# Kernel tuning notes

Measured on AMD Instinct MI355X. Metric: run time of the kernel, lower is better.

The kernel has to match this reference:

```python
import jax, jax.numpy as jnp
import numpy as np
import math

B, S, D = 2, 2048, 2048
P = 4       # num_entangled_pairs
PW = 2      # num_interference_pathways
L = 2       # num_layers
STD = 0.02
EPS = 1e-5


def _layer_norm(x, g, b):
    m = jnp.mean(x, axis=-1, keepdims=True)
    v = jnp.mean(jnp.square(x - m), axis=-1, keepdims=True)
    return (x - m) * jax.lax.rsqrt(v + EPS) * g + b


def setup_inputs() -> dict:
    key = jax.random.key(0)
    ks = jax.random.split(key, 16)
    n = lambda k, shape: jax.random.normal(k, shape, dtype=jnp.float32) * STD
    inp = {
        "x": jax.random.normal(ks[0], (B, S, D), dtype=jnp.float32),
        # superposition layer
        "amp_w": n(ks[1], (D, D)), "amp_b": jnp.zeros((D,), jnp.float32),
        "ph_w": n(ks[2], (D, D)), "ph_b": jnp.zeros((D,), jnp.float32),
        # per-layer entanglement
        "ent_w": n(ks[3], (L, D, P * D)), "ent_b": jnp.zeros((L, P * D), jnp.float32),
        "ent_pw": n(ks[4], (L, P * D, D)), "ent_pb": jnp.zeros((L, D), jnp.float32),
        # per-layer interference pathways
        "path_w": n(ks[5], (L, PW, D, D)), "path_b": jnp.zeros((L, PW, D), jnp.float32),
        "phase": jax.random.normal(ks[6], (L, PW, D), dtype=jnp.float32),
        # layer norms (norm3 / norm4 of each layer)
        "ln3_g": jnp.ones((L, D), jnp.float32), "ln3_b": jnp.zeros((L, D), jnp.float32),
        "ln4_g": jnp.ones((L, D), jnp.float32), "ln4_b": jnp.zeros((L, D), jnp.float32),
    }
    return inp


def reference(x, amp_w, amp_b, ph_w, ph_b, ent_w, ent_b, ent_pw, ent_pb,
              path_w, path_b, phase, ln3_g, ln3_b, ln4_g, ln4_b):
    # QuantumSuperpositionLayer on the input
    amp = jax.nn.sigmoid(x @ amp_w + amp_b)
    ph = jnp.tanh(x @ ph_w + ph_b) * math.pi
    h = (jnp.cos(ph) + jnp.sin(ph)) * amp                      # [B,S,D]

    for l in range(L):
        # QuantumEntanglementLayer: expand to P*D then project back
        e = h @ ent_w[l] + ent_b[l]                            # [B,S,P*D]
        ent = e @ ent_pw[l] + ent_pb[l]                        # [B,S,D]
        h = _layer_norm(h + ent, ln3_g[l], ln3_b[l])

        # QuantumInterferenceLayer: sum over pathways with phase modulation
        t = jnp.einsum('bsd,pdf->pbsf', h, path_w[l]) + path_b[l][:, None, None, :]
        mod = jnp.cos(phase[l]) + jnp.sin(phase[l])            # [PW,D]
        interf = jnp.sum(t * mod[:, None, None, :], axis=0)   # [B,S,D]
        h = _layer_norm(h + interf, ln4_g[l], ln4_b[l])
    return h
```

## Files before the change

### kernel.cpp

```cpp
#include <hip/hip_runtime.h>
#include <cstdint>
#include <cstddef>

typedef unsigned short u16;
typedef short bf16x8 __attribute__((ext_vector_type(8)));
typedef float f32x4 __attribute__((ext_vector_type(4)));

__device__ __forceinline__ float bf2f(u16 v) {
  union { unsigned int u; float f; } x; x.u = ((unsigned int)v) << 16; return x.f;
}
__device__ __forceinline__ u16 f2bf(float f) {
  union { float f; unsigned int u; } x; x.f = f;
  unsigned int r = (x.u + 0x7fffu + ((x.u >> 16) & 1u)) >> 16;
  return (u16)r;
}

__device__ __forceinline__ void async16(const u16* g, u16* lds) {
  __builtin_amdgcn_global_load_lds(
      (const __attribute__((address_space(1))) void*)g,
      (__attribute__((address_space(3))) void*)lds, 16, 0, 0);
}

#define BM 256
#define BN 256
#define BK 64

#define VMW(n) asm volatile("s_waitcnt vmcnt(" #n ")" ::: "memory")
#define BAR() do { asm volatile("" ::: "memory"); \
                   __builtin_amdgcn_s_barrier(); \
                   asm volatile("" ::: "memory"); } while (0)

template <bool ACC>
__global__ __launch_bounds__(512, 2) void gemm_bt(
    const u16* __restrict__ A, int lda,
    const u16* __restrict__ Bt,
    const float* __restrict__ bias,
    u16* __restrict__ C, int ldc,
    int M, int N, int K)
{
  __shared__ __align__(16) u16 As[2][BM * BK];
  __shared__ __align__(16) u16 Bs[2][BN * BK];
  const int tid = threadIdx.x;
  const int w   = tid >> 6;
  const int l   = tid & 63;
  const int wm  = w >> 2;
  const int wn  = w & 3;
  const int tRow = l & 15;
  const int quad = l >> 4;
  const int s7 = tRow & 7;
  const int bm = blockIdx.x, bn = blockIdx.y;

  const int rsub = tid >> 3;
  const int cLog = (tid & 7) ^ (rsub & 7);
  const u16* ag[2][2]; const u16* bg[2][2];
  #pragma unroll
  for (int H = 0; H < 2; ++H) {
    #pragma unroll
    for (int j = 0; j < 2; ++j) {
      const int ra = H * 64 + j * 128 + rsub;
      ag[H][j] = A + (size_t)(bm * BM + ra) * lda + cLog * 8;
      const int p  = j * 64 + rsub;
      const int rb = (p & 31) + H * 32 + (p >> 5) * 64;
      bg[H][j] = Bt + (size_t)(bn * BN + rb) * K + cLog * 8;
    }
  }
  const int ldsW = w * 512;

  f32x4 acc[8][4] = {};
  bf16x8 af[4][2], bf0[2][2], bf1[2][2];

#define STAGE_A(H, NB) do { \
    async16(ag[H][0], &As[NB][(H) * 8192 + ldsW]); \
    async16(ag[H][1], &As[NB][(H) * 8192 + 4096 + ldsW]); \
    ag[H][0] += BK; ag[H][1] += BK; } while (0)
#define STAGE_B(H, NB) do { \
    async16(bg[H][0], &Bs[NB][(H) * 8192 + ldsW]); \
    async16(bg[H][1], &Bs[NB][(H) * 8192 + 4096 + ldsW]); \
    bg[H][0] += BK; bg[H][1] += BK; } while (0)
#define READ_A(CB, H) do { \
    _Pragma("unroll") \
    for (int mt = 0; mt < 4; ++mt) { \
      _Pragma("unroll") \
      for (int kk = 0; kk < 2; ++kk) \
        af[mt][kk] = *(const bf16x8*)&As[CB][(H) * 8192 + \
            (wm * 64 + mt * 16 + tRow) * 64 + (((kk * 4 + quad) ^ s7)) * 8]; \
    } } while (0)
#define READ_B(CB, H, BF) do { \
    _Pragma("unroll") \
    for (int nt = 0; nt < 2; ++nt) { \
      _Pragma("unroll") \
      for (int kk = 0; kk < 2; ++kk) \
        BF[nt][kk] = *(const bf16x8*)&Bs[CB][(H) * 8192 + \
            (wn * 32 + nt * 16 + tRow) * 64 + (((kk * 4 + quad) ^ s7)) * 8]; \
    } } while (0)
#define MFMA_BLK(BF, MI0, NI0) do { \
    __builtin_amdgcn_s_setprio(1); \
    _Pragma("unroll") \
    for (int mt = 0; mt < 4; ++mt) { \
      _Pragma("unroll") \
      for (int nt = 0; nt < 2; ++nt) { \
        _Pragma("unroll") \
        for (int kk = 0; kk < 2; ++kk) \
          acc[(MI0) + mt][(NI0) + nt] = __builtin_amdgcn_mfma_f32_16x16x32_bf16( \
              af[mt][kk], BF[nt][kk], acc[(MI0) + mt][(NI0) + nt], 0, 0, 0); \
      } } \
    __builtin_amdgcn_s_setprio(0); } while (0)

  STAGE_A(0, 0); STAGE_B(0, 0); STAGE_B(1, 0); STAGE_A(1, 0);
  VMW(4);
  BAR();

  const int NT = K / BK;
  for (int u = 0; u < NT - 1; ++u) {
    const int cb = u & 1, nb = cb ^ 1;
    READ_A(cb, 0); READ_B(cb, 0, bf0);
    STAGE_A(0, nb);
    VMW(4); BAR();
    MFMA_BLK(bf0, 0, 0);
    BAR();
    READ_B(cb, 1, bf1);
    STAGE_B(0, nb);
    VMW(4); BAR();
    MFMA_BLK(bf1, 0, 2);
    BAR();
    READ_A(cb, 1);
    STAGE_B(1, nb);
    VMW(4); BAR();
    MFMA_BLK(bf1, 4, 2);
    BAR();
    STAGE_A(1, nb);
    VMW(4); BAR();
    MFMA_BLK(bf0, 4, 0);
    BAR();
  }
  {
    const int cb = (NT - 1) & 1;
    READ_A(cb, 0); READ_B(cb, 0, bf0);
    VMW(2); BAR();
    MFMA_BLK(bf0, 0, 0);
    BAR();
    READ_B(cb, 1, bf1);
    VMW(0); BAR();
    MFMA_BLK(bf1, 0, 2);
    BAR();
    READ_A(cb, 1);
    BAR();
    MFMA_BLK(bf1, 4, 2);
    BAR();
    MFMA_BLK(bf0, 4, 0);
  }
#undef STAGE_A
#undef STAGE_B
#undef READ_A
#undef READ_B
#undef MFMA_BLK

  const int crow0 = bm * BM + wm * 128;
  const int ccol0 = bn * BN + wn * 64;
  #pragma unroll
  for (int ni = 0; ni < 4; ++ni) {
    int col = ccol0 + ni * 16 + tRow;
    float bv = ACC ? 0.f : bias[col];
    #pragma unroll
    for (int mi = 0; mi < 8; ++mi) {
      int r0 = crow0 + mi * 16 + quad * 4;
      #pragma unroll
      for (int r = 0; r < 4; ++r) {
        size_t idx = (size_t)(r0 + r) * ldc + col;
        float v = acc[mi][ni][r] + bv;
        if (ACC) v += bf2f(C[idx]);
        C[idx] = f2bf(v);
      }
    }
  }
}

__global__ __launch_bounds__(256) void transpose_f2bf(
    const float* __restrict__ src, u16* __restrict__ dst,
    int R, int C, int srcStride, int col0)
{
  __shared__ __align__(16) u16 tile[64][72];
  const int bx = blockIdx.x;
  const int by = blockIdx.y;
  const int t = threadIdx.x;
  const int r  = t >> 4;
  const int c4 = (t & 15) * 4;
  #pragma unroll
  for (int i = 0; i < 4; ++i) {
    int row = r + i * 16;
    f32x4 v = *(const f32x4*)&src[(size_t)(by * 64 + row) * srcStride + col0 + bx * 64 + c4];
    #pragma unroll
    for (int j = 0; j < 4; ++j) tile[row][c4 + j] = f2bf(v[j]);
  }
  __syncthreads();
  const int orow0 = t >> 3;
  const int oc8   = (t & 7) * 8;
  #pragma unroll
  for (int i = 0; i < 2; ++i) {
    int orow = orow0 + i * 32;
    u16 tmp[8];
    #pragma unroll
    for (int j = 0; j < 8; ++j) tmp[j] = tile[oc8 + j][orow];
    *(uint4*)&dst[(size_t)(bx * 64 + orow) * R + by * 64 + oc8] = *(uint4*)tmp;
  }
}

__global__ void cvt_f2bf(const float* __restrict__ s, u16* __restrict__ d) {
  size_t i = ((size_t)blockIdx.x * 256 + threadIdx.x) * 8;
  f32x4 a = *(const f32x4*)&s[i];
  f32x4 b = *(const f32x4*)&s[i + 4];
  u16 o[8];
  #pragma unroll
  for (int j = 0; j < 4; ++j) { o[j] = f2bf(a[j]); o[j + 4] = f2bf(b[j]); }
  *(uint4*)&d[i] = *(uint4*)o;
}

__global__ void mod_k(const float* __restrict__ ph, float* __restrict__ m, int n) {
  int i = blockIdx.x * 256 + threadIdx.x;
  if (i < n) { float p = ph[i]; m[i] = cosf(p) + sinf(p); }
}

__global__ void concat2_k(const float* __restrict__ a, const float* __restrict__ b,
                          float* __restrict__ d, int n) {
  int i = blockIdx.x * 256 + threadIdx.x;
  if (i < n) { d[i] = a[i]; d[n + i] = b[i]; }
}

__global__ __launch_bounds__(256) void combine_path_k(
    const float* __restrict__ pw, const float* __restrict__ mod,
    u16* __restrict__ WcT, int D)
{
  __shared__ float tile[64][65];
  const int bx = blockIdx.x;
  const int by = blockIdx.y;
  const int t = threadIdx.x;
  const int r  = t >> 4;
  const int c4 = (t & 15) * 4;
  float acc[4][4];
  #pragma unroll
  for (int i = 0; i < 4; ++i)
    #pragma unroll
    for (int j = 0; j < 4; ++j) acc[i][j] = 0.f;
  for (int p = 0; p < 2; ++p) {
    float m[4];
    #pragma unroll
    for (int j = 0; j < 4; ++j) m[j] = mod[p * D + bx * 64 + c4 + j];
    #pragma unroll
    for (int i = 0; i < 4; ++i) {
      int d = by * 64 + r + i * 16;
      f32x4 v = *(const f32x4*)&pw[((size_t)p * D + d) * D + bx * 64 + c4];
      #pragma unroll
      for (int j = 0; j < 4; ++j) acc[i][j] += v[j] * m[j];
    }
  }
  #pragma unroll
  for (int i = 0; i < 4; ++i)
    #pragma unroll
    for (int j = 0; j < 4; ++j) tile[r + i * 16][c4 + j] = acc[i][j];
  __syncthreads();
  const int fo0 = t >> 3;
  const int oc8 = (t & 7) * 8;
  #pragma unroll
  for (int i = 0; i < 2; ++i) {
    int fo = fo0 + i * 32;
    u16 tmp[8];
    #pragma unroll
    for (int j = 0; j < 8; ++j) tmp[j] = f2bf(tile[oc8 + j][fo]);
    *(uint4*)&WcT[(size_t)(bx * 64 + fo) * D + by * 64 + oc8] = *(uint4*)tmp;
  }
}

__global__ void combine_bias_k(const float* __restrict__ pb, const float* __restrict__ mod,
                               float* __restrict__ bc, int D) {
  int f = blockIdx.x * 256 + threadIdx.x;
  if (f < D) bc[f] = pb[f] * mod[f] + pb[D + f] * mod[D + f];
}

__global__ __launch_bounds__(256) void superpose_k(
    const u16* __restrict__ zc, u16* __restrict__ h, int D)
{
  size_t idx = (size_t)blockIdx.x * 256 + threadIdx.x;
  int grpPerRow = D / 8;
  size_t row = idx / grpPerRow;
  int cg = (int)(idx % grpPerRow);
  size_t zbase = row * (size_t)(2 * D) + cg * 8;
  uint4 v1 = *(const uint4*)&zc[zbase];
  uint4 v2 = *(const uint4*)&zc[zbase + D];
  const u16* p1 = (const u16*)&v1;
  const u16* p2 = (const u16*)&v2;
  u16 o[8];
  #pragma unroll
  for (int j = 0; j < 8; ++j) {
    float a = bf2f(p1[j]);
    float p = bf2f(p2[j]);
    float amp = 1.f / (1.f + __expf(-a));
    float ph = 3.14159265358979323f * tanhf(p);
    float s, c;
    __sincosf(ph, &s, &c);
    o[j] = f2bf((c + s) * amp);
  }
  *(uint4*)&h[row * D + cg * 8] = *(uint4*)o;
}

template <bool F32OUT>
__global__ __launch_bounds__(256) void add_ln_k(
    const u16* __restrict__ hin, const u16* __restrict__ delta,
    const float* __restrict__ g, const float* __restrict__ b,
    void* __restrict__ outp, int D)
{
  const int row = blockIdx.x;
  const int t = threadIdx.x;
  const size_t base = (size_t)row * D;
  uint4 hv = *(const uint4*)&hin[base + t * 8];
  uint4 dv = *(const uint4*)&delta[base + t * 8];
  const u16* hp = (const u16*)&hv;
  const u16* dp = (const u16*)&dv;
  float x[8];
  float s = 0.f, s2 = 0.f;
  #pragma unroll
  for (int j = 0; j < 8; ++j) {
    x[j] = bf2f(hp[j]) + bf2f(dp[j]);
    s += x[j]; s2 += x[j] * x[j];
  }
  #pragma unroll
  for (int o = 32; o > 0; o >>= 1) {
    s  += __shfl_down(s, o, 64);
    s2 += __shfl_down(s2, o, 64);
  }
  __shared__ float ss[4], ss2[4];
  if ((t & 63) == 0) { ss[t >> 6] = s; ss2[t >> 6] = s2; }
  __syncthreads();
  float S  = ss[0] + ss[1] + ss[2] + ss[3];
  float S2 = ss2[0] + ss2[1] + ss2[2] + ss2[3];
  float mean = S / D;
  float var = S2 / D - mean * mean;
  float rstd = rsqrtf(var + 1e-5f);
  float y[8];
  #pragma unroll
  for (int j = 0; j < 8; ++j)
    y[j] = (x[j] - mean) * rstd * g[t * 8 + j] + b[t * 8 + j];
  if constexpr (F32OUT) {
    float* out = (float*)outp;
    f32x4 lo = {y[0], y[1], y[2], y[3]};
    f32x4 hi = {y[4], y[5], y[6], y[7]};
    *(f32x4*)&out[base + t * 8]     = lo;
    *(f32x4*)&out[base + t * 8 + 4] = hi;
  } else {
    u16* out = (u16*)outp;
    u16 o8[8];
    #pragma unroll
    for (int j = 0; j < 8; ++j) o8[j] = f2bf(y[j]);
    *(uint4*)&out[base + t * 8] = *(uint4*)o8;
  }
}

extern "C" void kernel_launch(void* const* d_in, const int* in_sizes, int n_in,
                              void* d_out, int out_size, void* d_ws, size_t ws_size,
                              hipStream_t stream) {
  const float* x      = (const float*)d_in[0];
  const float* amp_w  = (const float*)d_in[1];
  const float* amp_b  = (const float*)d_in[2];
  const float* ph_w   = (const float*)d_in[3];
  const float* ph_b   = (const float*)d_in[4];
  const float* ent_w  = (const float*)d_in[5];
  const float* ent_b  = (const float*)d_in[6];
  const float* ent_pw = (const float*)d_in[7];
  const float* ent_pb = (const float*)d_in[8];
  const float* path_w = (const float*)d_in[9];
  const float* path_b = (const float*)d_in[10];
  const float* phase  = (const float*)d_in[11];
  const float* ln3_g  = (const float*)d_in[12];
  const float* ln3_b  = (const float*)d_in[13];
  const float* ln4_g  = (const float*)d_in[14];
  const float* ln4_b  = (const float*)d_in[15];

  constexpr int D = 2048, PD = 8192, M = 4096, L = 2, PW = 2;
  constexpr int HPD = PD / 2;

  char* p = (char*)d_ws;
  float* modf = (float*)p; p += (size_t)L * PW * D * sizeof(float);
  float* bcf  = (float*)p; p += (size_t)2 * D * sizeof(float);
  p = (char*)d_ws + 65536;
  u16* h  = (u16*)p; p += (size_t)M * D * sizeof(u16);
  u16* t1 = (u16*)p; p += (size_t)M * D * sizeof(u16);
  u16* wT = (u16*)p; p += (size_t)HPD * D * sizeof(u16);
  u16* e  = (u16*)p; p += (size_t)M * PD * sizeof(u16);

  u16* xb = e;
  u16* zc = e + (size_t)M * D;

  dim3 b256(256);
  dim3 b512(512);

  mod_k<<<(L * PW * D) / 256, b256, 0, stream>>>(phase, modf, L * PW * D);
  cvt_f2bf<<<(M * D) / (256 * 8), b256, 0, stream>>>(x, xb);

  transpose_f2bf<<<dim3(D / 64, D / 64), b256, 0, stream>>>(amp_w, wT, D, D, D, 0);
  transpose_f2bf<<<dim3(D / 64, D / 64), b256, 0, stream>>>(ph_w, wT + (size_t)D * D, D, D, D, 0);
  concat2_k<<<D / 256, b256, 0, stream>>>(amp_b, ph_b, bcf, D);
  gemm_bt<false><<<dim3(M / BM, (2 * D) / BN), b512, 0, stream>>>(
      xb, D, wT, bcf, zc, 2 * D, M, 2 * D, D);
  superpose_k<<<(M * D) / (256 * 8), b256, 0, stream>>>(zc, h, D);

  for (int l = 0; l < L; ++l) {
    for (int s = 0; s < 2; ++s) {
      transpose_f2bf<<<dim3(HPD / 64, D / 64), b256, 0, stream>>>(
          ent_w + (size_t)l * D * PD, wT, D, HPD, PD, s * HPD);
      gemm_bt<false><<<dim3(M / BM, HPD / BN), b512, 0, stream>>>(
          h, D, wT, ent_b + (size_t)l * PD + s * HPD, e + s * HPD, PD, M, HPD, D);
    }
    for (int s = 0; s < 2; ++s) {
      transpose_f2bf<<<dim3(D / 64, HPD / 64), b256, 0, stream>>>(
          ent_pw + (size_t)l * PD * D + (size_t)s * HPD * D, wT, HPD, D, D, 0);
      if (s == 0)
        gemm_bt<false><<<dim3(M / BM, D / BN), b512, 0, stream>>>(
            e, PD, wT, ent_pb + (size_t)l * D, t1, D, M, D, HPD);
      else
        gemm_bt<true><<<dim3(M / BM, D / BN), b512, 0, stream>>>(
            e + HPD, PD, wT, bcf , t1, D, M, D, HPD);
    }
    add_ln_k<false><<<M, b256, 0, stream>>>(h, t1, ln3_g + (size_t)l * D, ln3_b + (size_t)l * D, h, D);
    combine_path_k<<<dim3(D / 64, D / 64), b256, 0, stream>>>(
        path_w + (size_t)l * PW * D * D, modf + (size_t)l * PW * D, wT, D);
    combine_bias_k<<<D / 256, b256, 0, stream>>>(path_b + (size_t)l * PW * D, modf + (size_t)l * PW * D, bcf, D);
    gemm_bt<false><<<dim3(M / BM, D / BN), b512, 0, stream>>>(
        h, D, wT, bcf, t1, D, M, D, D);
    if (l == L - 1)
      add_ln_k<true><<<M, b256, 0, stream>>>(h, t1, ln4_g + (size_t)l * D, ln4_b + (size_t)l * D, d_out, D);
    else
      add_ln_k<false><<<M, b256, 0, stream>>>(h, t1, ln4_g + (size_t)l * D, ln4_b + (size_t)l * D, h, D);
  }
}
```

Baseline: 1.511 ms.

## Template GEMM on N-tile width and deepen async prefetch to two tiles ahead

Makes the GEMM tile width a template parameter and uses 128-wide N tiles for the M x 2048 output GEMMs, doubling grid size for better CU occupancy. The main loop is restructured so both LDS buffers are filled in the prologue and each tile's buffer is refilled after it is consumed, keeping two K-tiles of loads in flight with tuned vmcnt waits. Narrower tiles lower arithmetic intensity per block, and the deeper pipeline depends on correct wait counts.

```diff
diff --git a/kernel.cpp b/kernel.cpp
--- a/kernel.cpp
+++ b/kernel.cpp
@@ -21,16 +21,27 @@
       (__attribute__((address_space(3))) void*)lds, 16, 0, 0);
 }
 
-#define BM 256
-#define BN 256
-#define BK 64
-
-#define VMW(n) asm volatile("s_waitcnt vmcnt(" #n ")" ::: "memory")
+template <int N> __device__ __forceinline__ void vmw() {
+  if constexpr (N < 0) {}
+  else if constexpr (N == 0)  asm volatile("s_waitcnt vmcnt(0)" ::: "memory");
+  else if constexpr (N == 2)  asm volatile("s_waitcnt vmcnt(2)" ::: "memory");
+  else if constexpr (N == 3)  asm volatile("s_waitcnt vmcnt(3)" ::: "memory");
+  else if constexpr (N == 4)  asm volatile("s_waitcnt vmcnt(4)" ::: "memory");
+  else if constexpr (N == 6)  asm volatile("s_waitcnt vmcnt(6)" ::: "memory");
+  else if constexpr (N == 8)  asm volatile("s_waitcnt vmcnt(8)" ::: "memory");
+  else if constexpr (N == 9)  asm volatile("s_waitcnt vmcnt(9)" ::: "memory");
+  else if constexpr (N == 10) asm volatile("s_waitcnt vmcnt(10)" ::: "memory");
+  else if constexpr (N == 12) asm volatile("s_waitcnt vmcnt(12)" ::: "memory");
+}
+
 #define BAR() do { asm volatile("" ::: "memory"); \
                    __builtin_amdgcn_s_barrier(); \
                    asm volatile("" ::: "memory"); } while (0)
 
-template <bool ACC>
+#define BM 256
+#define BK 64
+
+template <bool ACC, int BNT>
 __global__ __launch_bounds__(512, 2) void gemm_bt(
     const u16* __restrict__ A, int lda,
     const u16* __restrict__ Bt,
@@ -38,8 +49,14 @@
     u16* __restrict__ C, int ldc,
     int M, int N, int K)
 {
+  constexpr int NIH   = BNT / 128;
+  constexpr int NI    = 2 * NIH;
+  constexpr int JB    = BNT / 128;
+  constexpr int BHALF = BNT * 32;
+
   __shared__ __align__(16) u16 As[2][BM * BK];
-  __shared__ __align__(16) u16 Bs[2][BN * BK];
+  __shared__ __align__(16) u16 Bs[2][BNT * BK];
+
   const int tid = threadIdx.x;
   const int w   = tid >> 6;
   const int l   = tid & 63;
@@ -52,31 +69,35 @@
 
   const int rsub = tid >> 3;
   const int cLog = (tid & 7) ^ (rsub & 7);
-  const u16* ag[2][2]; const u16* bg[2][2];
+  const u16* ag[2][2]; const u16* bg[2][JB];
   #pragma unroll
   for (int H = 0; H < 2; ++H) {
     #pragma unroll
     for (int j = 0; j < 2; ++j) {
       const int ra = H * 64 + j * 128 + rsub;
       ag[H][j] = A + (size_t)(bm * BM + ra) * lda + cLog * 8;
+    }
+    #pragma unroll
+    for (int j = 0; j < JB; ++j) {
       const int p  = j * 64 + rsub;
-      const int rb = (p & 31) + H * 32 + (p >> 5) * 64;
-      bg[H][j] = Bt + (size_t)(bn * BN + rb) * K + cLog * 8;
+      const int rb = (p / (16 * NIH)) * (32 * NIH) + H * (16 * NIH) + (p % (16 * NIH));
+      bg[H][j] = Bt + (size_t)(bn * BNT + rb) * K + cLog * 8;
     }
   }
   const int ldsW = w * 512;
 
-  f32x4 acc[8][4] = {};
-  bf16x8 af[4][2], bf0[2][2], bf1[2][2];
+  f32x4 acc[8][NI] = {};
+  bf16x8 af[4][2], bf0[NIH][2], bf1[NIH][2];
 
 #define STAGE_A(H, NB) do { \
     async16(ag[H][0], &As[NB][(H) * 8192 + ldsW]); \
     async16(ag[H][1], &As[NB][(H) * 8192 + 4096 + ldsW]); \
     ag[H][0] += BK; ag[H][1] += BK; } while (0)
 #define STAGE_B(H, NB) do { \
-    async16(bg[H][0], &Bs[NB][(H) * 8192 + ldsW]); \
-    async16(bg[H][1], &Bs[NB][(H) * 8192 + 4096 + ldsW]); \
-    bg[H][0] += BK; bg[H][1] += BK; } while (0)
+    _Pragma("unroll") \
+    for (int j = 0; j < JB; ++j) { \
+      async16(bg[H][j], &Bs[NB][(H) * BHALF + j * 4096 + ldsW]); \
+      bg[H][j] += BK; } } while (0)
 #define READ_A(CB, H) do { \
     _Pragma("unroll") \
     for (int mt = 0; mt < 4; ++mt) { \
@@ -87,18 +108,18 @@
     } } while (0)
 #define READ_B(CB, H, BF) do { \
     _Pragma("unroll") \
-    for (int nt = 0; nt < 2; ++nt) { \
+    for (int nt = 0; nt < NIH; ++nt) { \
       _Pragma("unroll") \
       for (int kk = 0; kk < 2; ++kk) \
-        BF[nt][kk] = *(const bf16x8*)&Bs[CB][(H) * 8192 + \
-            (wn * 32 + nt * 16 + tRow) * 64 + (((kk * 4 + quad) ^ s7)) * 8]; \
+        BF[nt][kk] = *(const bf16x8*)&Bs[CB][(H) * BHALF + \
+            (wn * 16 * NIH + nt * 16 + tRow) * 64 + (((kk * 4 + quad) ^ s7)) * 8]; \
     } } while (0)
 #define MFMA_BLK(BF, MI0, NI0) do { \
     __builtin_amdgcn_s_setprio(1); \
     _Pragma("unroll") \
     for (int mt = 0; mt < 4; ++mt) { \
       _Pragma("unroll") \
-      for (int nt = 0; nt < 2; ++nt) { \
+      for (int nt = 0; nt < NIH; ++nt) { \
         _Pragma("unroll") \
         for (int kk = 0; kk < 2; ++kk) \
           acc[(MI0) + mt][(NI0) + nt] = __builtin_amdgcn_mfma_f32_16x16x32_bf16( \
@@ -106,49 +127,51 @@
       } } \
     __builtin_amdgcn_s_setprio(0); } while (0)
 
+#define TILE(P0, P1, P3, DOSTAGE) do { \
+    const int cb = u & 1; \
+     \
+    READ_A(cb, 0); READ_B(cb, 0, bf0); \
+    vmw<P0>(); BAR(); \
+    MFMA_BLK(bf0, 0, 0); \
+    BAR(); \
+     \
+    READ_B(cb, 1, bf1); \
+    if (DOSTAGE) { STAGE_A(0, cb); STAGE_B(0, cb); } \
+    vmw<P1>(); BAR(); \
+    MFMA_BLK(bf1, 0, NIH); \
+    BAR(); \
+     \
+    READ_A(cb, 1); \
+    if (DOSTAGE) { STAGE_B(1, cb); } \
+    BAR(); \
+    MFMA_BLK(bf1, 4, NIH); \
+    BAR(); \
+     \
+    if (DOSTAGE) { STAGE_A(1, cb); } \
+    vmw<P3>(); BAR(); \
+    MFMA_BLK(bf0, 4, 0); \
+    BAR(); \
+  } while (0)
+
+  constexpr int PRO = (BNT == 256) ? 12 : 9;
+  constexpr int P0W = (BNT == 256) ? 10 : 8;
+  constexpr int P1W = (BNT == 256) ? 12 : 9;
+  constexpr int P3W = (BNT == 256) ? 12 : 9;
+  constexpr int T1W = (BNT == 256) ? 8 : 6;
+  constexpr int T3W = (BNT == 256) ? 4 : 3;
+
   STAGE_A(0, 0); STAGE_B(0, 0); STAGE_B(1, 0); STAGE_A(1, 0);
-  VMW(4);
+  STAGE_A(0, 1); STAGE_B(0, 1); STAGE_B(1, 1); STAGE_A(1, 1);
+  vmw<PRO>();
   BAR();
 
   const int NT = K / BK;
-  for (int u = 0; u < NT - 1; ++u) {
-    const int cb = u & 1, nb = cb ^ 1;
-    READ_A(cb, 0); READ_B(cb, 0, bf0);
-    STAGE_A(0, nb);
-    VMW(4); BAR();
-    MFMA_BLK(bf0, 0, 0);
-    BAR();
-    READ_B(cb, 1, bf1);
-    STAGE_B(0, nb);
-    VMW(4); BAR();
-    MFMA_BLK(bf1, 0, 2);
-    BAR();
-    READ_A(cb, 1);
-    STAGE_B(1, nb);
-    VMW(4); BAR();
-    MFMA_BLK(bf1, 4, 2);
-    BAR();
-    STAGE_A(1, nb);
-    VMW(4); BAR();
-    MFMA_BLK(bf0, 4, 0);
-    BAR();
-  }
-  {
-    const int cb = (NT - 1) & 1;
-    READ_A(cb, 0); READ_B(cb, 0, bf0);
-    VMW(2); BAR();
-    MFMA_BLK(bf0, 0, 0);
-    BAR();
-    READ_B(cb, 1, bf1);
-    VMW(0); BAR();
-    MFMA_BLK(bf1, 0, 2);
-    BAR();
-    READ_A(cb, 1);
-    BAR();
-    MFMA_BLK(bf1, 4, 2);
-    BAR();
-    MFMA_BLK(bf0, 4, 0);
-  }
+  int u = 0;
+  for (; u < NT - 2; ++u) { TILE(P0W, P1W, P3W, true); }
+  { TILE(P0W, T1W, T3W, false); ++u; }
+  { TILE(2, 0, -1, false); }
+
+#undef TILE
 #undef STAGE_A
 #undef STAGE_B
 #undef READ_A
@@ -156,9 +179,9 @@
 #undef MFMA_BLK
 
   const int crow0 = bm * BM + wm * 128;
-  const int ccol0 = bn * BN + wn * 64;
-  #pragma unroll
-  for (int ni = 0; ni < 4; ++ni) {
+  const int ccol0 = bn * BNT + wn * (NIH * 32);
+  #pragma unroll
+  for (int ni = 0; ni < NI; ++ni) {
     int col = ccol0 + ni * 16 + tRow;
     float bv = ACC ? 0.f : bias[col];
     #pragma unroll
@@ -398,7 +421,7 @@
   transpose_f2bf<<<dim3(D / 64, D / 64), b256, 0, stream>>>(amp_w, wT, D, D, D, 0);
   transpose_f2bf<<<dim3(D / 64, D / 64), b256, 0, stream>>>(ph_w, wT + (size_t)D * D, D, D, D, 0);
   concat2_k<<<D / 256, b256, 0, stream>>>(amp_b, ph_b, bcf, D);
-  gemm_bt<false><<<dim3(M / BM, (2 * D) / BN), b512, 0, stream>>>(
+  gemm_bt<false, 256><<<dim3(M / BM, (2 * D) / 256), b512, 0, stream>>>(
       xb, D, wT, bcf, zc, 2 * D, M, 2 * D, D);
   superpose_k<<<(M * D) / (256 * 8), b256, 0, stream>>>(zc, h, D);
 
@@ -406,24 +429,24 @@
     for (int s = 0; s < 2; ++s) {
       transpose_f2bf<<<dim3(HPD / 64, D / 64), b256, 0, stream>>>(
           ent_w + (size_t)l * D * PD, wT, D, HPD, PD, s * HPD);
-      gemm_bt<false><<<dim3(M / BM, HPD / BN), b512, 0, stream>>>(
+      gemm_bt<false, 256><<<dim3(M / BM, HPD / 256), b512, 0, stream>>>(
           h, D, wT, ent_b + (size_t)l * PD + s * HPD, e + s * HPD, PD, M, HPD, D);
     }
     for (int s = 0; s < 2; ++s) {
       transpose_f2bf<<<dim3(D / 64, HPD / 64), b256, 0, stream>>>(
           ent_pw + (size_t)l * PD * D + (size_t)s * HPD * D, wT, HPD, D, D, 0);
       if (s == 0)
-        gemm_bt<false><<<dim3(M / BM, D / BN), b512, 0, stream>>>(
+        gemm_bt<false, 128><<<dim3(M / BM, D / 128), b512, 0, stream>>>(
             e, PD, wT, ent_pb + (size_t)l * D, t1, D, M, D, HPD);
       else
-        gemm_bt<true><<<dim3(M / BM, D / BN), b512, 0, stream>>>(
+        gemm_bt<true, 128><<<dim3(M / BM, D / 128), b512, 0, stream>>>(
             e + HPD, PD, wT, bcf , t1, D, M, D, HPD);
     }
     add_ln_k<false><<<M, b256, 0, stream>>>(h, t1, ln3_g + (size_t)l * D, ln3_b + (size_t)l * D, h, D);
     combine_path_k<<<dim3(D / 64, D / 64), b256, 0, stream>>>(
         path_w + (size_t)l * PW * D * D, modf + (size_t)l * PW * D, wT, D);
     combine_bias_k<<<D / 256, b256, 0, stream>>>(path_b + (size_t)l * PW * D, modf + (size_t)l * PW * D, bcf, D);
-    gemm_bt<false><<<dim3(M / BM, D / BN), b512, 0, stream>>>(
+    gemm_bt<false, 128><<<dim3(M / BM, D / 128), b512, 0, stream>>>(
         h, D, wT, bcf, t1, D, M, D, D);
     if (l == L - 1)
       add_ln_k<true><<<M, b256, 0, stream>>>(h, t1, ln4_g + (size_t)l * D, ln4_b + (size_t)l * D, d_out, D);
```

Result: faster. 1.418 ms (-6.2%).
